# Kernel tuning notes

Measured on AMD Instinct MI355X. Metric: run time of the kernel, lower is better.

The kernel has to match this reference:

```python
import jax, jax.numpy as jnp
import numpy as np

B, S, L = 128, 8192, 32


def setup_inputs() -> dict:
    key = jax.random.key(0)
    k1, k2, k3, k4, k5 = jax.random.split(key, 5)
    logits = jax.random.normal(k1, (B, S, L), dtype=jnp.float32)
    labels = jax.random.randint(k2, (B, S), 0, L)
    loss_mask = jnp.ones((B, S), dtype=bool)
    transitions = jax.random.normal(k3, (L, L), dtype=jnp.float32) * 0.1
    start_transition = jax.random.normal(k4, (L,), dtype=jnp.float32) * 0.1
    end_transition = jax.random.normal(k5, (L,), dtype=jnp.float32) * 0.1
    return {"logits": logits, "labels": labels, "loss_mask": loss_mask,
            "transitions": transitions, "start_transition": start_transition,
            "end_transition": end_transition}


def _denominator(logits, mask, transitions, start_transition, end_transition):
    # forward algorithm in log-space; carry: (B, L) alpha scores
    init = start_transition + logits[:, 0]

    def step(score, xs):
        logits_t, mask_t = xs  # (B, L), (B,)
        # (B, prev L, next L) -> logsumexp over prev
        score_t = jax.nn.logsumexp(
            score[:, :, None] + transitions[None] + logits_t[:, None, :], axis=1)
        score = jnp.where(mask_t[:, None], score_t, score)
        return score, None

    xs = (jnp.swapaxes(logits[:, 1:], 0, 1), jnp.swapaxes(mask[:, 1:], 0, 1))
    final, _ = jax.lax.scan(step, init, xs)
    return jax.nn.logsumexp(final + end_transition, axis=1)  # (B,)


def _numerator(logits, labels, mask, transitions, start_transition, end_transition):
    maskf = mask.astype(logits.dtype)
    arange_b = jnp.arange(logits.shape[0])
    # emission scores for t in [0, S-2], gathered at gold labels
    emis = jnp.take_along_axis(logits[:, :-1], labels[:, :-1, None], axis=2)[..., 0]
    trans_sc = transitions[labels[:, :-1], labels[:, 1:]]  # (B, S-1)
    score = start_transition[labels[:, 0]] + jnp.sum(
        emis * maskf[:, :-1] + trans_sc * maskf[:, 1:], axis=1)
    last_idx = mask.sum(axis=1).astype(jnp.int32) - 1
    last_labels = labels[arange_b, last_idx]
    score = score + logits[arange_b, -1, last_labels] * maskf[:, -1] \
            + end_transition[last_labels]
    return score  # (B,)


def reference(logits, labels, loss_mask, transitions, start_transition, end_transition):
    log_num = _numerator(logits, labels, loss_mask, transitions,
                         start_transition, end_transition)
    log_den = _denominator(logits, loss_mask, transitions,
                           start_transition, end_transition)
    llh = log_num - log_den
    return -jnp.mean(llh)  # reduction='mean'
```

## Files before the change

### kernel.cpp

```cpp
#include <hip/hip_runtime.h>
#include <hip/hip_bf16.h>


typedef float    f32x16 __attribute__((ext_vector_type(16)));
typedef float    f32x2  __attribute__((ext_vector_type(2)));
typedef __bf16   bf16x8 __attribute__((ext_vector_type(8)));
typedef unsigned uint4v __attribute__((ext_vector_type(4)));
typedef unsigned u32x2  __attribute__((ext_vector_type(2)));

#if __has_builtin(__builtin_amdgcn_permlane32_swap)
#define HAVE_PLSWAP 1
#else
#define HAVE_PLSWAP 0
#endif

#define CRF_S 8192
#define CRF_B 128
#define CRF_C 128
#define CRF_LC 64
#define CRF_W 64
#define CRF_G 8

__device__ inline unsigned pk_hi16(float a, float b) {
    return __builtin_amdgcn_perm(__builtin_bit_cast(unsigned, b),
                                 __builtin_bit_cast(unsigned, a), 0x07060302u);
}

__device__ inline float fast_exp_m4(float x) {
#if __has_builtin(__builtin_amdgcn_exp2f)
    return __builtin_amdgcn_exp2f(__builtin_fmaf(x, 1.44269504f, -5.77078016f));
#else
    return __expf(x - 4.0f);
#endif
}

__device__ inline f32x16 mfma_pair(bf16x8 Alo, bf16x8 Blo,
                                   bf16x8 Ahi, bf16x8 Bhi) {
    f32x16 z;
    asm("s_nop 1\n\t"
        "v_mfma_f32_32x32x16_bf16 %0, %1, %2, 0\n\t"
        "v_mfma_f32_32x32x16_bf16 %0, %3, %4, %0\n\t"
        "s_nop 7\n\t"
        "s_nop 7\n\t"
        "s_nop 2"
        : "=&v"(z)
        : "v"(Alo), "v"(Blo), "v"(Ahi), "v"(Bhi));
    return z;
}

__device__ inline void crf_renorm(f32x16& acc, float& off) {
    float mx = fmaxf(acc[0], acc[1]);
#pragma unroll
    for (int r = 2; r < 16; ++r) mx = fmaxf(mx, acc[r]);
#pragma unroll
    for (int d = 1; d < 64; d <<= 1) mx = fmaxf(mx, __shfl_xor(mx, d, 64));
    int bits = __builtin_bit_cast(int, mx);
    int e = ((bits >> 23) & 255) - 127;
    if (e < -100) e = 0;
    if (e > 120) e = 120;
    float scale = __builtin_bit_cast(float, (127 - e) << 23);
    acc *= scale;
    off += (float)e * 0.6931471805599453f;
}

__device__ inline void repack_B(const f32x16& acc, int h, bf16x8& Blo, bf16x8& Bhi) {
    unsigned p[8];
#pragma unroll
    for (int i = 0; i < 8; ++i) p[i] = pk_hi16(acc[2 * i], acc[2 * i + 1]);
#if HAVE_PLSWAP
    u32x2 r0 = __builtin_amdgcn_permlane32_swap(p[0], p[2], false, false);
    u32x2 r1 = __builtin_amdgcn_permlane32_swap(p[1], p[3], false, false);
    u32x2 r2 = __builtin_amdgcn_permlane32_swap(p[4], p[6], false, false);
    u32x2 r3 = __builtin_amdgcn_permlane32_swap(p[5], p[7], false, false);
    uint4v bl = {r0[0], r1[0], r0[1], r1[1]};
    uint4v bh = {r2[0], r3[0], r2[1], r3[1]};
#else
    unsigned q[8];
#pragma unroll
    for (int i = 0; i < 8; ++i) q[i] = (unsigned)__shfl_xor((int)p[i], 32, 64);
    bool hiw = (h != 0);
    uint4v bl = { hiw ? q[2] : p[0], hiw ? q[3] : p[1],
                  hiw ? p[2] : q[0], hiw ? p[3] : q[1] };
    uint4v bh = { hiw ? q[6] : p[4], hiw ? q[7] : p[5],
                  hiw ? p[6] : q[4], hiw ? p[7] : q[5] };
#endif
    Blo = __builtin_bit_cast(bf16x8, bl);
    Bhi = __builtin_bit_cast(bf16x8, bh);
}

__device__ inline void crf_step_mat(f32x16& acc, float v, int h,
                                    const f32x2* e2) {
    float ev = fast_exp_m4(v);
    f32x2 ev2 = {ev, ev};
    unsigned av[8];
#pragma unroll
    for (int i = 0; i < 8; ++i) {
        f32x2 m = e2[i] * ev2;
        av[i] = pk_hi16(m[0], m[1]);
    }
    bf16x8 Alo = __builtin_bit_cast(bf16x8, (uint4v){av[0], av[1], av[2], av[3]});
    bf16x8 Ahi = __builtin_bit_cast(bf16x8, (uint4v){av[4], av[5], av[6], av[7]});
    bf16x8 Blo, Bhi;
    repack_B(acc, h, Blo, Bhi);
    acc = mfma_pair(Alo, Blo, Ahi, Bhi);
}

__global__ __launch_bounds__(256) void crf_phase1(
    const float* __restrict__ logits, const int* __restrict__ labels,
    const float* __restrict__ trans, unsigned* __restrict__ mat16,
    float* __restrict__ ws_off, float* __restrict__ ws_num2) {
    const int S = CRF_S, Lc = CRF_LC, C = CRF_C;
    int lane = threadIdx.x & 63, j = lane & 31, h = lane >> 5;
    int wid = blockIdx.x * 4 + (threadIdx.x >> 6);
    int b = wid >> 6, k = wid & 63;
    int cA = k, cB = k + CRF_W;
    const float BIAS = 1.001953125f;

    f32x2 e2[8];
#pragma unroll
    for (int i = 0; i < 4; ++i) {
        e2[i][0]     = __expf(trans[(8 * h + 2 * i) * 32 + j]) * BIAS;
        e2[i][1]     = __expf(trans[(8 * h + 2 * i + 1) * 32 + j]) * BIAS;
        e2[4 + i][0] = __expf(trans[(16 + 8 * h + 2 * i) * 32 + j]) * BIAS;
        e2[4 + i][1] = __expf(trans[(16 + 8 * h + 2 * i + 1) * 32 + j]) * BIAS;
    }

    f32x16 accA = {}, accB = {};
#pragma unroll
    for (int r = 0; r < 16; ++r) {
        int row = (r & 3) + 8 * (r >> 2) + 4 * h;
        float idv = (row == j) ? 1.0f : 0.0f;
        accA[r] = idv; accB[r] = idv;
    }

    int startA = (cA == 0) ? 1 : 0;
    int nA = Lc - startA, nB = Lc;
    int tA0 = cA * Lc + startA, tB0 = cB * Lc;
    const float* pA = logits + ((size_t)b * S + (size_t)tA0) * 32;
    const float* pB = logits + ((size_t)b * S + (size_t)tB0) * 32;
    const int* lab = labels + (size_t)b * S;

    float a0 = pA[j], a1 = pA[32 + j], a2 = pA[64 + j];
    float b0 = pB[j], b1 = pB[32 + j], b2 = pB[64 + j];

    int l0A = lab[tA0],     l1A = lab[tA0 + 1],
        l2A = lab[tA0 + 2], l3A = lab[tA0 + 3];
    int l0B = lab[tB0],     l1B = lab[tB0 + 1],
        l2B = lab[tB0 + 2], l3B = lab[tB0 + 3];

    int lpA = lab[tA0 - 1], lpB = lab[tB0 - 1];
    float tq0A = trans[lpA * 32 + l0A], tq1A = trans[l0A * 32 + l1A];
    float tq0B = trans[lpB * 32 + l0B], tq1B = trans[l0B * 32 + l1B];

    float emis = 0.0f, tr = 0.0f;

    for (int s = 0; s < Lc - 1; ++s) {
        {
            tr += tq0A;
            emis += (lane == l0A) ? a0 : 0.0f;
            crf_step_mat(accA, a0, h, e2);
            tq0A = tq1A;
            tq1A = trans[l1A * 32 + l2A];
            l0A = l1A; l1A = l2A; l2A = l3A;
            int lx = s + 4; if (lx > nA - 1) lx = nA - 1;
            l3A = lab[tA0 + lx];
            a0 = a1; a1 = a2;
            int ix = s + 3; if (ix > nA - 1) ix = nA - 1;
            a2 = pA[(size_t)ix * 32 + j];
        }
        {
            tr += tq0B;
            emis += (lane == l0B) ? b0 : 0.0f;
            crf_step_mat(accB, b0, h, e2);
            tq0B = tq1B;
            tq1B = trans[l1B * 32 + l2B];
            l0B = l1B; l1B = l2B; l2B = l3B;
            int lx = s + 4; if (lx > nB - 1) lx = nB - 1;
            l3B = lab[tB0 + lx];
            b0 = b1; b1 = b2;
            int ix = s + 3; if (ix > nB - 1) ix = nB - 1;
            b2 = pB[(size_t)ix * 32 + j];
        }
    }
    if (nA == Lc) {
        tr += tq0A;
        emis += (lane == l0A) ? a0 : 0.0f;
        crf_step_mat(accA, a0, h, e2);
    }
    {
        tr += tq0B;
        emis += (lane == l0B) ? b0 : 0.0f;
        crf_step_mat(accB, b0, h, e2);
    }

    float offA = 0.0f, offB = 0.0f;
    crf_renorm(accA, offA); offA += 4.0f * (float)nA;
    crf_renorm(accB, offB); offB += 4.0f * (float)nB;

    unsigned* baseA = mat16 + (size_t)(b * C + cA) * 512;
    unsigned* baseB = mat16 + (size_t)(b * C + cB) * 512;
#pragma unroll
    for (int i = 0; i < 8; ++i) {
        int re = ((2 * i) & 3) + 8 * ((2 * i) >> 2) + 4 * h;
        baseA[j * 16 + (re >> 1)] = pk_hi16(accA[2 * i], accA[2 * i + 1]);
        baseB[j * 16 + (re >> 1)] = pk_hi16(accB[2 * i], accB[2 * i + 1]);
    }
#pragma unroll
    for (int d = 1; d < 64; d <<= 1) emis += __shfl_xor(emis, d, 64);
    if (lane == 0) {
        ws_off[b * C + cA] = offA;
        ws_off[b * C + cB] = offB;
        ws_num2[b * CRF_W + k] = emis + tr;
    }
}

__global__ __launch_bounds__(256) void crf_phase2a(
    const unsigned* __restrict__ mat16, const float* __restrict__ ws_off,
    float* __restrict__ gmat, float* __restrict__ goff) {
    int lane = threadIdx.x & 63;
    int wid = blockIdx.x * 4 + (threadIdx.x >> 6);
    int b = wid >> 3, g = wid & 7;
    int j = lane & 31, h = lane >> 5;
    int cpg = CRF_C / CRF_G;

    f32x16 acc = {};
#pragma unroll
    for (int r = 0; r < 16; ++r) {
        int row = (r & 3) + 8 * (r >> 2) + 4 * h;
        acc[r] = (row == j) ? 1.0f : 0.0f;
    }
    float off = 0.0f;
    int cbase = b * CRF_C + g * cpg;

    for (int s = cpg - 1; s >= 0; --s) {
        const uint4v* Ap = (const uint4v*)(mat16 + (size_t)(cbase + s) * 512);
        bf16x8 Alo = __builtin_bit_cast(bf16x8, Ap[j * 4 + h]);
        bf16x8 Ahi = __builtin_bit_cast(bf16x8, Ap[j * 4 + 2 + h]);
        bf16x8 Blo, Bhi;
        repack_B(acc, h, Blo, Bhi);
        acc = mfma_pair(Alo, Blo, Ahi, Bhi);
        off += ws_off[cbase + s];
    }
    crf_renorm(acc, off);
    float* base = gmat + (size_t)(b * CRF_G + g) * 1024;
#pragma unroll
    for (int r = 0; r < 16; ++r) {
        int row = (r & 3) + 8 * (r >> 2) + 4 * h;
        base[j * 32 + row] = acc[r];
    }
    if (lane == 0) goff[b * CRF_G + g] = off;
}

__global__ __launch_bounds__(64) void crf_phase2b(
    const float* __restrict__ logits, const int* __restrict__ labels,
    const float* __restrict__ startT, const float* __restrict__ endT,
    const float* __restrict__ gmat, const float* __restrict__ goff,
    const float* __restrict__ ws_num2, float* __restrict__ out) {
    const int S = CRF_S, G = CRF_G;
    int b = blockIdx.x;
    int lane = threadIdx.x & 63;
    int j = lane & 31;
    __shared__ __align__(16) float sp[2][32];

    float logit0 = logits[(size_t)b * S * 32 + j];
    float sv = startT[j], evv = endT[j];
    float vlog = sv + logit0;
    float m = vlog;
#pragma unroll
    for (int d = 1; d < 32; d <<= 1) m = fmaxf(m, __shfl_xor(m, d, 64));
    float p = __expf(vlog - m);
    float accl = m;

    int buf = 0;
    if (lane < 32) sp[0][j] = p;
    __syncthreads();

    const float* mat = gmat + (size_t)b * G * 1024 + j * 32;
    float4 mreg[8];
#pragma unroll
    for (int i = 0; i < 8; ++i) mreg[i] = ((const float4*)mat)[i];

    for (int c = 0; c < G; ++c) {
        const float* nmat = mat + (size_t)((c + 1 < G) ? c + 1 : c) * 1024;
        float4 nreg[8];
#pragma unroll
        for (int i = 0; i < 8; ++i) nreg[i] = ((const float4*)nmat)[i];

        const float4* spv = (const float4*)sp[buf];
        float vnew = 0.0f;
#pragma unroll
        for (int i = 0; i < 8; ++i) {
            float4 pv = spv[i];
            vnew += pv.x * mreg[i].x + pv.y * mreg[i].y +
                    pv.z * mreg[i].z + pv.w * mreg[i].w;
        }
        float mx = vnew;
#pragma unroll
        for (int d = 1; d < 32; d <<= 1) mx = fmaxf(mx, __shfl_xor(mx, d, 64));
        int bits = __builtin_bit_cast(int, mx);
        int e = ((bits >> 23) & 255) - 127;
        if (e < -100) e = 0;
        if (e > 120) e = 120;
        float scale = __builtin_bit_cast(float, (127 - e) << 23);
        p = vnew * scale;
        accl += (float)e * 0.6931471805599453f + goff[b * G + c];

        buf ^= 1;
        if (lane < 32) sp[buf][j] = p;
        __syncthreads();
#pragma unroll
        for (int i = 0; i < 8; ++i) mreg[i] = nreg[i];
    }

    float tj = p * __expf(evv);
    float ssum = tj;
#pragma unroll
    for (int d = 1; d < 32; d <<= 1) ssum += __shfl_xor(ssum, d, 64);
    float den = accl + __logf(ssum);

    float nsum = ws_num2[b * CRF_W + lane];
#pragma unroll
    for (int d = 1; d < 64; d <<= 1) nsum += __shfl_xor(nsum, d, 64);

    int lab0 = labels[(size_t)b * S];
    int labL = labels[(size_t)b * S + S - 1];
    float num = nsum + __shfl(sv, lab0, 64) + __shfl(logit0, lab0, 64) +
                __shfl(evv, labL, 64);
    if (lane == 0) atomicAdd(out, -(num - den) * (1.0f / (float)CRF_B));
}

extern "C" void kernel_launch(void* const* d_in, const int* in_sizes, int n_in,
                              void* d_out, int out_size, void* d_ws, size_t ws_size,
                              hipStream_t stream) {
    const float* logits = (const float*)d_in[0];
    const int*   labels = (const int*)d_in[1];
    const float* trans  = (const float*)d_in[3];
    const float* startT = (const float*)d_in[4];
    const float* endT   = (const float*)d_in[5];
    float* out = (float*)d_out;

    const int B = CRF_B, C = CRF_C;
    unsigned* mat16 = (unsigned*)d_ws;
    float* gmat   = (float*)((char*)d_ws + (size_t)B * C * 2048);
    float* ws_off = gmat + (size_t)B * CRF_G * 1024;
    float* goff   = ws_off + (size_t)B * C;
    float* ws_num2 = goff + B * CRF_G;

    hipMemsetAsync(out, 0, sizeof(float), stream);

    crf_phase1<<<dim3(B * CRF_W / 4), dim3(256), 0, stream>>>(
        logits, labels, trans, mat16, ws_off, ws_num2);
    crf_phase2a<<<dim3(B * CRF_G / 4), dim3(256), 0, stream>>>(
        mat16, ws_off, gmat, goff);
    crf_phase2b<<<dim3(B), dim3(64), 0, stream>>>(
        logits, labels, startT, endT, gmat, goff, ws_num2, out);
}
```

Measured before the change: 315.6 us.

## Fuse phase2a into phase2b, drop memset, use uniform pointers in phase1

Merges the group-matrix product kernel and the final sequential chain kernel into one kernel: eight waves per batch compute the group matrices into shared memory, then one wave runs the chain from LDS. The output zeroing moves into phase1, removing the memset launch. Phase1 also gains a clamp-free main loop with scalar base pointers and 32-bit incremented offsets to cut address arithmetic. This removes two launches and a global round-trip of the group matrices. The cost is 512-thread blocks where seven waves sit idle during the serial tail.

```diff
diff --git a/kernel.cpp b/kernel.cpp
--- a/kernel.cpp
+++ b/kernel.cpp
@@ -20,6 +20,19 @@
 #define CRF_LC 64
 #define CRF_W 64
 #define CRF_G 8
+
+__device__ inline const float* uf_fptr(const float* p) {
+    unsigned long long u = (unsigned long long)p;
+    unsigned lo = __builtin_amdgcn_readfirstlane((unsigned)u);
+    unsigned hi = __builtin_amdgcn_readfirstlane((unsigned)(u >> 32));
+    return (const float*)(((unsigned long long)hi << 32) | lo);
+}
+__device__ inline const int* uf_iptr(const int* p) {
+    unsigned long long u = (unsigned long long)p;
+    unsigned lo = __builtin_amdgcn_readfirstlane((unsigned)u);
+    unsigned hi = __builtin_amdgcn_readfirstlane((unsigned)(u >> 32));
+    return (const int*)(((unsigned long long)hi << 32) | lo);
+}
 
 __device__ inline unsigned pk_hi16(float a, float b) {
     return __builtin_amdgcn_perm(__builtin_bit_cast(unsigned, b),
@@ -108,7 +121,8 @@
 __global__ __launch_bounds__(256) void crf_phase1(
     const float* __restrict__ logits, const int* __restrict__ labels,
     const float* __restrict__ trans, unsigned* __restrict__ mat16,
-    float* __restrict__ ws_off, float* __restrict__ ws_num2) {
+    float* __restrict__ ws_off, float* __restrict__ ws_num2,
+    float* __restrict__ outz) {
     const int S = CRF_S, Lc = CRF_LC, C = CRF_C;
     int lane = threadIdx.x & 63, j = lane & 31, h = lane >> 5;
     int wid = blockIdx.x * 4 + (threadIdx.x >> 6);
@@ -116,6 +130,8 @@
     int cA = k, cB = k + CRF_W;
     const float BIAS = 1.001953125f;
 
+    if (blockIdx.x == 0 && threadIdx.x == 0) *outz = 0.0f;
+
     f32x2 e2[8];
 #pragma unroll
     for (int i = 0; i < 4; ++i) {
@@ -136,12 +152,14 @@
     int startA = (cA == 0) ? 1 : 0;
     int nA = Lc - startA, nB = Lc;
     int tA0 = cA * Lc + startA, tB0 = cB * Lc;
-    const float* pA = logits + ((size_t)b * S + (size_t)tA0) * 32;
-    const float* pB = logits + ((size_t)b * S + (size_t)tB0) * 32;
-    const int* lab = labels + (size_t)b * S;
-
-    float a0 = pA[j], a1 = pA[32 + j], a2 = pA[64 + j];
-    float b0 = pB[j], b1 = pB[32 + j], b2 = pB[64 + j];
+    const float* pA = uf_fptr(logits + ((size_t)b * S + (size_t)tA0) * 32);
+    const float* pB = uf_fptr(logits + ((size_t)b * S + (size_t)tB0) * 32);
+    const int* lab = uf_iptr(labels + (size_t)b * S);
+
+    unsigned aoff = (unsigned)j, boff = (unsigned)j;
+    float a0 = pA[aoff], a1 = pA[aoff + 32], a2 = pA[aoff + 64];
+    float b0 = pB[boff], b1 = pB[boff + 32], b2 = pB[boff + 64];
+    aoff += 96; boff += 96;
 
     int l0A = lab[tA0],     l1A = lab[tA0 + 1],
         l2A = lab[tA0 + 2], l3A = lab[tA0 + 3];
@@ -154,7 +172,35 @@
 
     float emis = 0.0f, tr = 0.0f;
 
-    for (int s = 0; s < Lc - 1; ++s) {
+    int nmin = (nA < nB) ? nA : nB;
+    int M = nmin - 5;
+    int s = 0;
+#pragma unroll 2
+    for (; s < M; ++s) {
+        {
+            tr += tq0A;
+            emis += (lane == l0A) ? a0 : 0.0f;
+            crf_step_mat(accA, a0, h, e2);
+            tq0A = tq1A;
+            tq1A = trans[l1A * 32 + l2A];
+            l0A = l1A; l1A = l2A; l2A = l3A;
+            l3A = lab[tA0 + s + 4];
+            a0 = a1; a1 = a2;
+            a2 = pA[aoff]; aoff += 32;
+        }
+        {
+            tr += tq0B;
+            emis += (lane == l0B) ? b0 : 0.0f;
+            crf_step_mat(accB, b0, h, e2);
+            tq0B = tq1B;
+            tq1B = trans[l1B * 32 + l2B];
+            l0B = l1B; l1B = l2B; l2B = l3B;
+            l3B = lab[tB0 + s + 4];
+            b0 = b1; b1 = b2;
+            b2 = pB[boff]; boff += 32;
+        }
+    }
+    for (; s < Lc - 1; ++s) {
         {
             tr += tq0A;
             emis += (lane == l0A) ? a0 : 0.0f;
@@ -166,7 +212,7 @@
             l3A = lab[tA0 + lx];
             a0 = a1; a1 = a2;
             int ix = s + 3; if (ix > nA - 1) ix = nA - 1;
-            a2 = pA[(size_t)ix * 32 + j];
+            a2 = pA[(unsigned)ix * 32 + j];
         }
         {
             tr += tq0B;
@@ -179,7 +225,7 @@
             l3B = lab[tB0 + lx];
             b0 = b1; b1 = b2;
             int ix = s + 3; if (ix > nB - 1) ix = nB - 1;
-            b2 = pB[(size_t)ix * 32 + j];
+            b2 = pB[(unsigned)ix * 32 + j];
         }
     }
     if (nA == Lc) {
@@ -214,53 +260,50 @@
     }
 }
 
-__global__ __launch_bounds__(256) void crf_phase2a(
-    const unsigned* __restrict__ mat16, const float* __restrict__ ws_off,
-    float* __restrict__ gmat, float* __restrict__ goff) {
-    int lane = threadIdx.x & 63;
-    int wid = blockIdx.x * 4 + (threadIdx.x >> 6);
-    int b = wid >> 3, g = wid & 7;
-    int j = lane & 31, h = lane >> 5;
-    int cpg = CRF_C / CRF_G;
-
-    f32x16 acc = {};
-#pragma unroll
-    for (int r = 0; r < 16; ++r) {
-        int row = (r & 3) + 8 * (r >> 2) + 4 * h;
-        acc[r] = (row == j) ? 1.0f : 0.0f;
-    }
-    float off = 0.0f;
-    int cbase = b * CRF_C + g * cpg;
-
-    for (int s = cpg - 1; s >= 0; --s) {
-        const uint4v* Ap = (const uint4v*)(mat16 + (size_t)(cbase + s) * 512);
-        bf16x8 Alo = __builtin_bit_cast(bf16x8, Ap[j * 4 + h]);
-        bf16x8 Ahi = __builtin_bit_cast(bf16x8, Ap[j * 4 + 2 + h]);
-        bf16x8 Blo, Bhi;
-        repack_B(acc, h, Blo, Bhi);
-        acc = mfma_pair(Alo, Blo, Ahi, Bhi);
-        off += ws_off[cbase + s];
-    }
-    crf_renorm(acc, off);
-    float* base = gmat + (size_t)(b * CRF_G + g) * 1024;
-#pragma unroll
-    for (int r = 0; r < 16; ++r) {
-        int row = (r & 3) + 8 * (r >> 2) + 4 * h;
-        base[j * 32 + row] = acc[r];
-    }
-    if (lane == 0) goff[b * CRF_G + g] = off;
-}
-
-__global__ __launch_bounds__(64) void crf_phase2b(
+__global__ __launch_bounds__(512) void crf_phase2(
     const float* __restrict__ logits, const int* __restrict__ labels,
     const float* __restrict__ startT, const float* __restrict__ endT,
-    const float* __restrict__ gmat, const float* __restrict__ goff,
+    const unsigned* __restrict__ mat16, const float* __restrict__ ws_off,
     const float* __restrict__ ws_num2, float* __restrict__ out) {
     const int S = CRF_S, G = CRF_G;
     int b = blockIdx.x;
+    int wv = threadIdx.x >> 6;
     int lane = threadIdx.x & 63;
-    int j = lane & 31;
+    int j = lane & 31, h = lane >> 5;
+    const int cpg = CRF_C / CRF_G;
+
+    __shared__ __align__(16) float smat[CRF_G][1024];
+    __shared__ float soff[CRF_G];
     __shared__ __align__(16) float sp[2][32];
+
+    {
+        f32x16 acc = {};
+#pragma unroll
+        for (int r = 0; r < 16; ++r) {
+            int row = (r & 3) + 8 * (r >> 2) + 4 * h;
+            acc[r] = (row == j) ? 1.0f : 0.0f;
+        }
+        float off = 0.0f;
+        int cbase = b * CRF_C + wv * cpg;
+        for (int s2 = cpg - 1; s2 >= 0; --s2) {
+            const uint4v* Ap = (const uint4v*)(mat16 + (size_t)(cbase + s2) * 512);
+            bf16x8 Alo = __builtin_bit_cast(bf16x8, Ap[j * 4 + h]);
+            bf16x8 Ahi = __builtin_bit_cast(bf16x8, Ap[j * 4 + 2 + h]);
+            bf16x8 Blo, Bhi;
+            repack_B(acc, h, Blo, Bhi);
+            acc = mfma_pair(Alo, Blo, Ahi, Bhi);
+            off += ws_off[cbase + s2];
+        }
+        crf_renorm(acc, off);
+#pragma unroll
+        for (int r = 0; r < 16; ++r) {
+            int row = (r & 3) + 8 * (r >> 2) + 4 * h;
+            smat[wv][j * 32 + row] = acc[r];
+        }
+        if (lane == 0) soff[wv] = off;
+    }
+    __syncthreads();
+    if (wv != 0) return;
 
     float logit0 = logits[(size_t)b * S * 32 + j];
     float sv = startT[j], evv = endT[j];
@@ -273,26 +316,16 @@
 
     int buf = 0;
     if (lane < 32) sp[0][j] = p;
-    __syncthreads();
-
-    const float* mat = gmat + (size_t)b * G * 1024 + j * 32;
-    float4 mreg[8];
-#pragma unroll
-    for (int i = 0; i < 8; ++i) mreg[i] = ((const float4*)mat)[i];
 
     for (int c = 0; c < G; ++c) {
-        const float* nmat = mat + (size_t)((c + 1 < G) ? c + 1 : c) * 1024;
-        float4 nreg[8];
-#pragma unroll
-        for (int i = 0; i < 8; ++i) nreg[i] = ((const float4*)nmat)[i];
-
+        const float* mat = &smat[c][j * 32];
         const float4* spv = (const float4*)sp[buf];
         float vnew = 0.0f;
 #pragma unroll
         for (int i = 0; i < 8; ++i) {
+            float4 mv = ((const float4*)mat)[i];
             float4 pv = spv[i];
-            vnew += pv.x * mreg[i].x + pv.y * mreg[i].y +
-                    pv.z * mreg[i].z + pv.w * mreg[i].w;
+            vnew += pv.x * mv.x + pv.y * mv.y + pv.z * mv.z + pv.w * mv.w;
         }
         float mx = vnew;
 #pragma unroll
@@ -303,13 +336,10 @@
         if (e > 120) e = 120;
         float scale = __builtin_bit_cast(float, (127 - e) << 23);
         p = vnew * scale;
-        accl += (float)e * 0.6931471805599453f + goff[b * G + c];
+        accl += (float)e * 0.6931471805599453f + soff[c];
 
         buf ^= 1;
         if (lane < 32) sp[buf][j] = p;
-        __syncthreads();
-#pragma unroll
-        for (int i = 0; i < 8; ++i) mreg[i] = nreg[i];
     }
 
     float tj = p * __expf(evv);
@@ -341,17 +371,11 @@
 
     const int B = CRF_B, C = CRF_C;
     unsigned* mat16 = (unsigned*)d_ws;
-    float* gmat   = (float*)((char*)d_ws + (size_t)B * C * 2048);
-    float* ws_off = gmat + (size_t)B * CRF_G * 1024;
-    float* goff   = ws_off + (size_t)B * C;
-    float* ws_num2 = goff + B * CRF_G;
-
-    hipMemsetAsync(out, 0, sizeof(float), stream);
+    float* ws_off = (float*)((char*)d_ws + (size_t)B * C * 2048);
+    float* ws_num2 = ws_off + (size_t)B * C;
 
     crf_phase1<<<dim3(B * CRF_W / 4), dim3(256), 0, stream>>>(
-        logits, labels, trans, mat16, ws_off, ws_num2);
-    crf_phase2a<<<dim3(B * CRF_G / 4), dim3(256), 0, stream>>>(
-        mat16, ws_off, gmat, goff);
-    crf_phase2b<<<dim3(B), dim3(64), 0, stream>>>(
-        logits, labels, startT, endT, gmat, goff, ws_num2, out);
-}
+        logits, labels, trans, mat16, ws_off, ws_num2, out);
+    crf_phase2<<<dim3(B), dim3(512), 0, stream>>>(
+        logits, labels, startT, endT, mat16, ws_off, ws_num2, out);
+}
```

After: 311.0 us. About the same (-1.5%).
